# Performance work log

Measured on AMD Instinct MI355X. Metric: run time of the kernel, lower is better.

## Reference

```python
import jax, jax.numpy as jnp
import numpy as np

B, Q, H = 1, 2048, 2048
NH, NKV, HD = 16, 8, 128
PAST = 2048
EPS = 1e-6


def rotate_half(x):
    x1, x2 = x[..., : x.shape[-1] // 2], x[..., x.shape[-1] // 2 :]
    return jnp.concatenate((-x2, x1), axis=-1)


def rms_norm(x, w, eps=EPS):
    var = jnp.mean(jnp.square(x.astype(jnp.float32)), axis=-1, keepdims=True)
    return (x * jax.lax.rsqrt(var + eps)) * w


def setup_inputs() -> dict:
    key = jax.random.key(0)
    ks = jax.random.split(key, 8)
    hidden_states = jax.random.normal(ks[0], (B, Q, H), jnp.float32)
    # RoPE tables for positions [PAST, PAST+Q)
    inv_freq = 1.0 / (1000000.0 ** (np.arange(0, HD, 2, dtype=np.float32) / HD))
    pos = np.arange(PAST, PAST + Q, dtype=np.float32)
    freqs = np.outer(pos, inv_freq)  # [Q, HD/2]
    emb = np.concatenate([freqs, freqs], axis=-1)  # [Q, HD]
    cos = jnp.asarray(np.cos(emb))[None].repeat(B, 0)
    sin = jnp.asarray(np.sin(emb))[None].repeat(B, 0)
    # causal additive mask over kv_len = PAST + Q
    q_idx = np.arange(Q)[:, None] + PAST
    kv_idx = np.arange(PAST + Q)[None, :]
    mask = np.where(kv_idx <= q_idx, 0.0, -1e9).astype(np.float32)
    attention_mask = jnp.asarray(mask)[None, None]  # [1,1,Q,PAST+Q]
    s = 1.0 / np.sqrt(H)
    return {
        "hidden_states": hidden_states,
        "cos": cos,
        "sin": sin,
        "attention_mask": attention_mask,
        "past_key": jax.random.normal(ks[1], (B, NKV, PAST, HD), jnp.float32),
        "past_value": jax.random.normal(ks[2], (B, NKV, PAST, HD), jnp.float32),
        "Wq": jax.random.normal(ks[3], (NH * HD, H), jnp.float32) * s,
        "Wk": jax.random.normal(ks[4], (NKV * HD, H), jnp.float32) * s,
        "Wv": jax.random.normal(ks[5], (NKV * HD, H), jnp.float32) * s,
        "Wo": jax.random.normal(ks[6], (NH * HD, NH * HD), jnp.float32) * s,
        "q_norm_w": jnp.ones((HD,), jnp.float32),
        "k_norm_w": jnp.ones((HD,), jnp.float32),
    }


def reference(hidden_states, cos, sin, attention_mask, past_key, past_value,
              Wq, Wk, Wv, Wo, q_norm_w, k_norm_w):
    bsz, q_len, _ = hidden_states.shape
    scaling = HD ** -0.5
    n_rep = NH // NKV

    q = jnp.einsum("bsh,dh->bsd", hidden_states, Wq).reshape(bsz, q_len, NH, HD).transpose(0, 2, 1, 3)
    k = jnp.einsum("bsh,dh->bsd", hidden_states, Wk).reshape(bsz, q_len, NKV, HD).transpose(0, 2, 1, 3)
    v = jnp.einsum("bsh,dh->bsd", hidden_states, Wv).reshape(bsz, q_len, NKV, HD).transpose(0, 2, 1, 3)

    q = rms_norm(q, q_norm_w)
    k = rms_norm(k, k_norm_w)

    c = cos[:, None]  # [B,1,Q,HD]
    s = sin[:, None]
    q = q * c + rotate_half(q) * s
    k = k * c + rotate_half(k) * s

    k_all = jnp.concatenate([past_key, k], axis=2)    # [B,NKV,PAST+Q,HD]
    v_all = jnp.concatenate([past_value, v], axis=2)
    new_key = k_all[:, :, -q_len:, :]
    new_value = v_all[:, :, -q_len:, :]

    kv_len = k_all.shape[2]
    k_rep = jnp.broadcast_to(k_all[:, :, None], (bsz, NKV, n_rep, kv_len, HD)).reshape(bsz, NH, kv_len, HD)
    v_rep = jnp.broadcast_to(v_all[:, :, None], (bsz, NKV, n_rep, kv_len, HD)).reshape(bsz, NH, kv_len, HD)

    scores = jnp.einsum("bhqd,bhkd->bhqk", q, k_rep) * scaling + attention_mask
    probs = jax.nn.softmax(scores.astype(jnp.float32), axis=-1).astype(q.dtype)
    out = jnp.einsum("bhqk,bhkd->bhqd", probs, v_rep)
    out = out.transpose(0, 2, 1, 3).reshape(bsz, q_len, NH * HD)
    out = jnp.einsum("bsd,hd->bsh", out, Wo)
    return out, new_key, new_value
```

## Files before the change

kernel.cpp:

```cpp
#include <hip/hip_runtime.h>
#include <hip/hip_bf16.h>

typedef __bf16 bf16_t;
typedef __bf16 bf16x8 __attribute__((ext_vector_type(8)));
typedef float f32x4 __attribute__((ext_vector_type(4)));

#define NH 16
#define NKV 8
#define HD 128
#define QLEN 2048
#define PASTLEN 2048
#define KVLEN 4096
#define NKOFF 4194304UL
#define NVOFF 6291456UL
#define SM_C1 0.12751741f
#define SM_C2 (-28.853900817779268f)

__device__ __forceinline__ void async16(const void* g, void* l) {
  __builtin_amdgcn_global_load_lds(
      (const __attribute__((address_space(1))) unsigned int*)g,
      (__attribute__((address_space(3))) unsigned int*)l, 16, 0, 0);
}

__device__ __forceinline__ bool detect_f32(const void* qw) {
  return *(const unsigned*)qw == 0x3F800000u;
}

__device__ __forceinline__ float ld1(const void* p, size_t i, bool f32) {
  return f32 ? ((const float*)p)[i] : (float)((const bf16_t*)p)[i];
}
__device__ __forceinline__ void st1(void* p, size_t i, bool f32, float v) {
  if (f32) ((float*)p)[i] = v; else ((bf16_t*)p)[i] = (bf16_t)v;
}
template <bool F32>
__device__ __forceinline__ uint4 ld8cvt(const void* p, size_t i) {
  if constexpr (!F32) {
    return *(const uint4*)((const bf16_t*)p + i);
  } else {
    const float* f = (const float*)p + i;
    float4 f0 = *(const float4*)f;
    float4 f1 = *(const float4*)(f + 4);
    union { bf16_t h[8]; uint4 u; } r;
    r.h[0] = (bf16_t)f0.x; r.h[1] = (bf16_t)f0.y; r.h[2] = (bf16_t)f0.z; r.h[3] = (bf16_t)f0.w;
    r.h[4] = (bf16_t)f1.x; r.h[5] = (bf16_t)f1.y; r.h[6] = (bf16_t)f1.z; r.h[7] = (bf16_t)f1.w;
    return r.u;
  }
}
__device__ __forceinline__ unsigned bfbits(float v) {
  bf16_t h = (bf16_t)v;
  union { bf16_t h; unsigned short u; } x; x.h = h;
  return (unsigned)x.u;
}

__global__ __launch_bounds__(256) void k_cvt4(
    const float* __restrict__ s0, const float* __restrict__ s1,
    const float* __restrict__ s2, const float* __restrict__ s3,
    bf16_t* __restrict__ d0, bf16_t* __restrict__ d1,
    bf16_t* __restrict__ d2, bf16_t* __restrict__ d3,
    const void* __restrict__ qw)
{
  if (!detect_f32(qw)) return;
  const int ten = blockIdx.y;
  const float* s; bf16_t* d; size_t n;
  switch (ten) {
    case 0:  s = s0; d = d0; n = 4194304; break;
    case 1:  s = s1; d = d1; n = 4194304; break;
    case 2:  s = s2; d = d2; n = 2097152; break;
    default: s = s3; d = d3; n = 2097152; break;
  }
  const size_t i = ((size_t)blockIdx.x * 256 + threadIdx.x) * 8;
  if (i >= n) return;
  uint4 v = ld8cvt<true>(s, i);
  *(uint4*)(d + i) = v;
}
__global__ __launch_bounds__(256) void k_cvt1(
    const float* __restrict__ s, bf16_t* __restrict__ d, const void* __restrict__ qw)
{
  if (!detect_f32(qw)) return;
  const size_t i = ((size_t)blockIdx.x * 256 + threadIdx.x) * 8;
  uint4 v = ld8cvt<true>(s, i);
  *(uint4*)(d + i) = v;
}

__device__ __forceinline__ void gemm_acc(
    const bf16_t* __restrict__ A, const bf16_t* __restrict__ B,
    int lda, int ldb, int m0, int n0, int K,
    bf16_t (*As)[4096], bf16_t (*Bs)[4096], f32x4 (*acc)[4])
{
  const int tid  = threadIdx.x;
  const int lane = tid & 63;
  const int w    = tid >> 6;
  const int wm   = w >> 1, wn = w & 1;
  const int qid  = lane & 15, quad = lane >> 4;

  const int r4 = tid >> 2;
  const int sg = (tid & 3) * 8;
  const size_t a0 = (size_t)(m0 + r4) * lda + sg;
  const size_t a1 = a0 + (size_t)64 * lda;
  const size_t b0 = (size_t)(n0 + r4) * ldb + sg;
  const size_t b1 = b0 + (size_t)64 * ldb;
  const int lo0 = tid * 8;
  const int lo1 = 2048 + tid * 8;

  auto stage = [&](int k0, int buf) {
    async16(A + a0 + k0, As[buf] + lo0);
    async16(A + a1 + k0, As[buf] + lo1);
    async16(B + b0 + k0, Bs[buf] + lo0);
    async16(B + b1 + k0, Bs[buf] + lo1);
  };

  stage(0, 0);

  for (int k0 = 0; k0 < K; k0 += 32) {
    const int cur = (k0 >> 5) & 1;
    if (k0 + 32 < K) {
      stage(k0 + 32, cur ^ 1);
      asm volatile("s_waitcnt vmcnt(4)" ::: "memory");
    } else {
      asm volatile("s_waitcnt vmcnt(0)" ::: "memory");
    }
    __builtin_amdgcn_s_barrier();

    bf16x8 af[4], bfr[4];
#pragma unroll
    for (int i = 0; i < 4; i++)
      af[i] = *(const bf16x8*)(As[cur] + (size_t)(wm * 64 + i * 16 + qid) * 32 + quad * 8);
#pragma unroll
    for (int j = 0; j < 4; j++)
      bfr[j] = *(const bf16x8*)(Bs[cur] + (size_t)(wn * 64 + j * 16 + qid) * 32 + quad * 8);
#pragma unroll
    for (int i = 0; i < 4; i++)
#pragma unroll
      for (int j = 0; j < 4; j++)
        acc[i][j] = __builtin_amdgcn_mfma_f32_16x16x32_bf16(af[i], bfr[j], acc[i][j], 0, 0, 0);

    __builtin_amdgcn_s_barrier();
  }
}

__global__ __launch_bounds__(256) void k_gemm_qkv(
    const void* __restrict__ hs, const void* __restrict__ Wq,
    const void* __restrict__ Wk, const void* __restrict__ Wv,
    const bf16_t* __restrict__ hsb, const bf16_t* __restrict__ Wqb,
    const bf16_t* __restrict__ Wkb, const bf16_t* __restrict__ Wvb,
    const void* __restrict__ cs, const void* __restrict__ sn,
    const void* __restrict__ qw, const void* __restrict__ kw,
    bf16_t* __restrict__ qb, bf16_t* __restrict__ kc, void* __restrict__ dout)
{
  __shared__ __align__(16) char smem[67072];
  bf16_t (*As)[4096] = (bf16_t(*)[4096])smem;
  bf16_t (*Bs)[4096] = (bf16_t(*)[4096])(smem + 16384);
  float (*xs)[129]   = (float(*)[129])smem;
  float (*rsum)[128] = (float(*)[128])(smem + 66048);

  const bool f = detect_f32(qw);
  const bf16_t* A = f ? hsb : (const bf16_t*)hs;
  const int bx = blockIdx.x, by = blockIdx.y;
  const bf16_t* B; int n0;
  if (bx < 16)      { B = f ? Wqb : (const bf16_t*)Wq; n0 = bx * 128; }
  else if (bx < 24) { B = f ? Wkb : (const bf16_t*)Wk; n0 = (bx - 16) * 128; }
  else              { B = f ? Wvb : (const bf16_t*)Wv; n0 = (bx - 24) * 128; }

  f32x4 acc[4][4] = {};
  gemm_acc(A, B, 2048, 2048, by * 128, n0, 2048, As, Bs, acc);

  const int tid = threadIdx.x, lane = tid & 63, w = tid >> 6;
  const int wm = w >> 1, wn = w & 1, qid = lane & 15, quad = lane >> 4;

  if (bx >= 24) {
    const int h = bx - 24;
#pragma unroll
    for (int i = 0; i < 4; i++)
#pragma unroll
      for (int j = 0; j < 4; j++) {
        const int rl = wm * 64 + i * 16 + quad * 4;
        const int d  = wn * 64 + j * 16 + qid;
#pragma unroll
        for (int r = 0; r < 4; r++) {
          const int s = by * 128 + rl + r;
          st1(dout, NVOFF + ((size_t)h * QLEN + s) * HD + d, f, acc[i][j][r]);
        }
      }
    return;
  }

  float rs[4][4];
#pragma unroll
  for (int i = 0; i < 4; i++)
#pragma unroll
    for (int r = 0; r < 4; r++) {
      float v = 0.f;
#pragma unroll
      for (int j = 0; j < 4; j++) v += acc[i][j][r] * acc[i][j][r];
#pragma unroll
      for (int o = 1; o < 16; o <<= 1) v += __shfl_xor(v, o, 64);
      rs[i][r] = v;
    }
#pragma unroll
  for (int i = 0; i < 4; i++)
#pragma unroll
    for (int j = 0; j < 4; j++) {
      const int rl = wm * 64 + i * 16 + quad * 4;
      const int d  = wn * 64 + j * 16 + qid;
#pragma unroll
      for (int r = 0; r < 4; r++) xs[rl + r][d] = acc[i][j][r];
    }
  if (qid == 0) {
#pragma unroll
    for (int i = 0; i < 4; i++)
#pragma unroll
      for (int r = 0; r < 4; r++)
        rsum[wn][wm * 64 + i * 16 + quad * 4 + r] = rs[i][r];
  }
  __syncthreads();
  const void* wgt = (bx < 16) ? qw : kw;
#pragma unroll
  for (int i = 0; i < 4; i++)
#pragma unroll
    for (int r = 0; r < 4; r++) {
      const int rl = wm * 64 + i * 16 + quad * 4 + r;
      const int s  = by * 128 + rl;
      const float inv = rsqrtf((rsum[0][rl] + rsum[1][rl]) * (1.0f / 128.0f) + 1e-6f);
#pragma unroll
      for (int j = 0; j < 4; j++) {
        const int d = wn * 64 + j * 16 + qid;
        const float x  = acc[i][j][r];
        const float xp = xs[rl][d ^ 64];
        const float y  = x  * inv * ld1(wgt, d, f);
        const float yp = xp * inv * ld1(wgt, d ^ 64, f);
        const float cv = ld1(cs, (size_t)s * HD + d, f);
        const float sv = ld1(sn, (size_t)s * HD + d, f);
        const float o  = (d < 64) ? y * cv - yp * sv : y * cv + yp * sv;
        if (bx < 16) {
          qb[(size_t)s * 2048 + bx * HD + d] = (bf16_t)o;
        } else {
          const int hk = bx - 16;
          st1(dout, NKOFF + ((size_t)hk * QLEN + s) * HD + d, f, o);
          kc[((size_t)hk * KVLEN + PASTLEN + s) * HD + d] = (bf16_t)o;
        }
      }
    }
}

__global__ __launch_bounds__(256) void k_gemm_o(
    const bf16_t* __restrict__ aout, const void* __restrict__ Wo,
    const bf16_t* __restrict__ Wob, void* __restrict__ dout,
    const void* __restrict__ qw)
{
  __shared__ bf16_t As[2][4096];
  __shared__ bf16_t Bs[2][4096];
  const bool f = detect_f32(qw);
  const bf16_t* B = f ? Wob : (const bf16_t*)Wo;
  f32x4 acc[4][4] = {};
  gemm_acc(aout, B, 2048, 2048, blockIdx.y * 128, blockIdx.x * 128, 2048, As, Bs, acc);

  const int tid = threadIdx.x, lane = tid & 63, w = tid >> 6;
  const int wm = w >> 1, wn = w & 1, qid = lane & 15, quad = lane >> 4;
#pragma unroll
  for (int i = 0; i < 4; i++)
#pragma unroll
    for (int j = 0; j < 4; j++) {
      const int rr = blockIdx.y * 128 + wm * 64 + i * 16 + quad * 4;
      const int cc = blockIdx.x * 128 + wn * 64 + j * 16 + qid;
#pragma unroll
      for (int r = 0; r < 4; r++)
        st1(dout, (size_t)(rr + r) * 2048 + cc, f, acc[i][j][r]);
    }
}

template <bool F>
__device__ __forceinline__ void prep_body(
    const void* __restrict__ pk, const void* __restrict__ pv,
    const void* __restrict__ dout,
    bf16_t* __restrict__ kc, bf16_t* __restrict__ vt,
    unsigned (*tile)[65])
{
  const int tid = threadIdx.x;
  const int hk = blockIdx.x >> 5, kvt = blockIdx.x & 31;
  const int kv0 = kvt * 128;

  if (kv0 < PASTLEN) {
    const size_t base = ((size_t)hk * PASTLEN + kv0) * HD;
    bf16_t* dst = kc + ((size_t)hk * KVLEN + kv0) * HD;
#pragma unroll
    for (int p = 0; p < 8; p++) {
      const int id = p * 256 + tid;
      const int r = id >> 4, c8 = (id & 15) * 8;
      uint4 vv = ld8cvt<F>(pk, base + (size_t)r * HD + c8);
      *(uint4*)(dst + (size_t)r * HD + c8) = vv;
    }
  }

  const void* src; size_t base;
  if (kv0 < PASTLEN) { src = pv;   base = ((size_t)hk * PASTLEN + kv0) * HD; }
  else               { src = dout; base = NVOFF + ((size_t)hk * QLEN + (kv0 - PASTLEN)) * HD; }
#pragma unroll
  for (int p = 0; p < 4; p++) {
    const int id = p * 256 + tid;
    const int r = id >> 4, e8 = (id & 15) * 8;
    if constexpr (!F) {
      uint4 a = *(const uint4*)((const bf16_t*)src + base + (size_t)(2 * r) * HD + e8);
      uint4 b = *(const uint4*)((const bf16_t*)src + base + (size_t)(2 * r + 1) * HD + e8);
      unsigned av[4] = {a.x, a.y, a.z, a.w}, bv[4] = {b.x, b.y, b.z, b.w};
#pragma unroll
      for (int q = 0; q < 4; q++) {
        tile[e8 + 2 * q][r]     = (av[q] & 0xffffu) | (bv[q] << 16);
        tile[e8 + 2 * q + 1][r] = (av[q] >> 16)     | (bv[q] & 0xffff0000u);
      }
    } else {
      const float* fa = (const float*)src + base + (size_t)(2 * r) * HD + e8;
      const float* fb = (const float*)src + base + (size_t)(2 * r + 1) * HD + e8;
#pragma unroll
      for (int e = 0; e < 8; e++)
        tile[e8 + e][r] = bfbits(fa[e]) | (bfbits(fb[e]) << 16);
    }
  }
  __syncthreads();
#pragma unroll
  for (int p = 0; p < 8; p++) {
    const int id = p * 256 + tid;
    const int e = id >> 4, c4 = (id & 15) * 4;
    uint4 wv;
    if (c4 & 8) {
      wv.x = tile[e][c4 + 2]; wv.y = tile[e][c4 + 3]; wv.z = tile[e][c4];     wv.w = tile[e][c4 + 1];
    } else {
      wv.x = tile[e][c4];     wv.y = tile[e][c4 + 1]; wv.z = tile[e][c4 + 2]; wv.w = tile[e][c4 + 3];
    }
    *(uint4*)(vt + ((size_t)hk * HD + e) * KVLEN + kv0 + c4 * 2) = wv;
  }
}
__global__ __launch_bounds__(256) void k_prep_kv(
    const void* __restrict__ pk, const void* __restrict__ pv,
    const void* __restrict__ dout,
    bf16_t* __restrict__ kc, bf16_t* __restrict__ vt, const void* __restrict__ qw)
{
  __shared__ unsigned tile[128][65];
  if (detect_f32(qw)) prep_body<true>(pk, pv, dout, kc, vt, tile);
  else                prep_body<false>(pk, pv, dout, kc, vt, tile);
}

__global__ __launch_bounds__(256, 2) void k_attn(
    const bf16_t* __restrict__ qb, const bf16_t* __restrict__ kc,
    const bf16_t* __restrict__ vt, bf16_t* __restrict__ aout)
{
  __shared__ bf16_t ks[2][64 * 128];
  __shared__ bf16_t vs[2][128 * 64];
  __shared__ float  lsx[2][64];

  const int tid = threadIdx.x, lane = tid & 63, w = tid >> 6;
  const int qid = lane & 15, quad = lane >> 4;
  const int qg = w & 1;
  const int kh = w >> 1;
  const int bx = blockIdx.x;
  const int h  = ((bx & 7) << 1) | (bx >> 3);
  const int hk = h >> 1;
  const int by = blockIdx.y;
  const int qt = (by < 16) ? by : 47 - by;
  const int q0 = qt * 64;

  bf16x8 qf[2][4];
#pragma unroll
  for (int i = 0; i < 2; i++)
#pragma unroll
    for (int kst = 0; kst < 4; kst++)
      qf[i][kst] = *(const bf16x8*)(qb + (size_t)(q0 + qg * 32 + i * 16 + qid) * 2048
                                       + h * HD + kst * 32 + quad * 8);

  f32x4 Oacc[2][8] = {};
  f32x4 lacc[2] = {};

  union { unsigned short u[8]; bf16x8 v; } onesu;
#pragma unroll
  for (int e = 0; e < 8; e++) onesu.u[e] = 0x3F80;
  const bf16x8 onesv = onesu.v;

  const int J = quad >> 1;
  int bpa[4];
#pragma unroll
  for (int s = 0; s < 4; s++)
    bpa[s] = 4 * (qid + 16 * ((2 * quad + ((s >> 1) ^ J)) & 3));

  const bf16_t* kbase = kc + (size_t)hk * KVLEN * HD;
  const bf16_t* vbase = vt + (size_t)hk * HD * KVLEN;
  const int r16 = tid >> 4, ksg = tid & 15;
  const int r8  = tid >> 3, vsg = tid & 7;
  const int nt = qt + 33;

  auto stage = [&](int t, int buf) {
    const int kv0 = t * 64;
#pragma unroll
    for (int c = 0; c < 4; c++) {
      const int kr = c * 16 + r16;
      async16(kbase + (size_t)(kv0 + kr) * HD + ((ksg ^ (kr & 7)) * 8),
              &ks[buf][(size_t)(c * 256 + tid) * 8]);
    }
#pragma unroll
    for (int c = 0; c < 4; c++) {
      const int vr = c * 32 + r8;
      async16(vbase + (size_t)vr * KVLEN + kv0 + ((vsg ^ (vr & 7)) * 8),
              &vs[buf][(size_t)(c * 256 + tid) * 8]);
    }
  };

  stage(0, 0);

  for (int t = 0; t < nt; ++t) {
    const int cur = t & 1;
    if (t + 1 < nt) {
      stage(t + 1, cur ^ 1);
      asm volatile("s_waitcnt vmcnt(8)" ::: "memory");
    } else {
      asm volatile("s_waitcnt vmcnt(0)" ::: "memory");
    }
    __builtin_amdgcn_s_barrier();

    const bf16_t* ksb = ks[cur];
    const bf16_t* vsb = vs[cur];
    const int kv0 = t * 64;

    f32x4 sf[2][2] = {};
    __builtin_amdgcn_s_setprio(1);
#pragma unroll
    for (int kst = 0; kst < 4; kst++) {
      bf16x8 kf[2];
#pragma unroll
      for (int j = 0; j < 2; j++)
        kf[j] = *(const bf16x8*)(ksb + (size_t)((kh * 2 + j) * 16 + qid) * 128
                                     + (((kst * 4 + quad) * 8) ^ ((qid & 7) * 8)));
#pragma unroll
      for (int i = 0; i < 2; i++)
#pragma unroll
        for (int j = 0; j < 2; j++)
          sf[i][j] = __builtin_amdgcn_mfma_f32_16x16x32_bf16(kf[j], qf[i][kst], sf[i][j], 0, 0, 0);
    }
    __builtin_amdgcn_s_setprio(0);

    const bool lastt = (t == nt - 1);
    bf16x8 pf[2];
#pragma unroll
    for (int i = 0; i < 2; i++) {
      const int qglob = q0 + qg * 32 + i * 16 + qid + PASTLEN;
      float pr[2][4];
#pragma unroll
      for (int j = 0; j < 2; j++) {
        const int kvb = kv0 + kh * 32 + j * 16 + quad * 4;
#pragma unroll
        for (int r = 0; r < 4; r++) {
          float v = fmaf(sf[i][j][r], SM_C1, SM_C2);
          if (lastt && (kvb + r) > qglob) v = -1e9f;
          pr[j][r] = exp2f(v);
        }
      }
      unsigned pk00, pk01, pk10, pk11;
      asm("v_cvt_pk_bf16_f32 %0, %1, %2" : "=v"(pk00) : "v"(pr[0][0]), "v"(pr[0][1]));
      asm("v_cvt_pk_bf16_f32 %0, %1, %2" : "=v"(pk01) : "v"(pr[0][2]), "v"(pr[0][3]));
      asm("v_cvt_pk_bf16_f32 %0, %1, %2" : "=v"(pk10) : "v"(pr[1][0]), "v"(pr[1][1]));
      asm("v_cvt_pk_bf16_f32 %0, %1, %2" : "=v"(pk11) : "v"(pr[1][2]), "v"(pr[1][3]));
      const bool qodd = (quad & 1) != 0;
      const unsigned reg0 = qodd ? pk10 : pk00;
      const unsigned reg1 = qodd ? pk11 : pk01;
      const unsigned reg2 = qodd ? pk00 : pk10;
      const unsigned reg3 = qodd ? pk01 : pk11;
      union { unsigned u[4]; bf16x8 v; } pu;
      pu.u[0] = (unsigned)__builtin_amdgcn_ds_bpermute(bpa[0], (int)reg0);
      pu.u[1] = (unsigned)__builtin_amdgcn_ds_bpermute(bpa[1], (int)reg1);
      pu.u[2] = (unsigned)__builtin_amdgcn_ds_bpermute(bpa[2], (int)reg2);
      pu.u[3] = (unsigned)__builtin_amdgcn_ds_bpermute(bpa[3], (int)reg3);
      pf[i] = pu.v;
    }

    __builtin_amdgcn_s_setprio(1);
    lacc[0] = __builtin_amdgcn_mfma_f32_16x16x32_bf16(pf[0], onesv, lacc[0], 0, 0, 0);
    lacc[1] = __builtin_amdgcn_mfma_f32_16x16x32_bf16(pf[1], onesv, lacc[1], 0, 0, 0);
#pragma unroll
    for (int n = 0; n < 8; n++) {
      bf16x8 vf = *(const bf16x8*)(vsb + (size_t)(n * 16 + qid) * 64
                                       + (((kh * 4 + quad) * 8) ^ ((qid & 7) * 8)));
      Oacc[0][n] = __builtin_amdgcn_mfma_f32_16x16x32_bf16(pf[0], vf, Oacc[0][n], 0, 0, 0);
      Oacc[1][n] = __builtin_amdgcn_mfma_f32_16x16x32_bf16(pf[1], vf, Oacc[1][n], 0, 0, 0);
    }
    __builtin_amdgcn_s_setprio(0);
    __builtin_amdgcn_s_barrier();
  }

  if (qid == 0) {
#pragma unroll
    for (int i = 0; i < 2; i++)
#pragma unroll
      for (int r = 0; r < 4; r++)
        lsx[kh][qg * 32 + i * 16 + quad * 4 + r] = lacc[i][r];
  }
  float* Osc = (float*)ks;
  if (kh == 1) {
#pragma unroll
    for (int i = 0; i < 2; i++)
#pragma unroll
      for (int n = 0; n < 8; n++)
#pragma unroll
        for (int r = 0; r < 4; r++)
          Osc[(size_t)qg * 4096 + (i * 16 + quad * 4 + r) * 128 + n * 16 + qid] = Oacc[i][n][r];
  }
  __syncthreads();
  if (kh == 0) {
#pragma unroll
    for (int i = 0; i < 2; i++) {
      float invl[4];
#pragma unroll
      for (int r = 0; r < 4; r++) {
        const int qq = qg * 32 + i * 16 + quad * 4 + r;
        invl[r] = 1.0f / (lsx[0][qq] + lsx[1][qq]);
      }
#pragma unroll
      for (int n = 0; n < 8; n++)
#pragma unroll
        for (int r = 0; r < 4; r++) {
          const float ot = Oacc[i][n][r]
            + Osc[(size_t)qg * 4096 + (i * 16 + quad * 4 + r) * 128 + n * 16 + qid];
          const int row = q0 + qg * 32 + i * 16 + quad * 4 + r;
          aout[(size_t)row * 2048 + h * HD + n * 16 + qid] = (bf16_t)(ot * invl[r]);
        }
    }
  }
}

extern "C" void kernel_launch(void* const* d_in, const int* in_sizes, int n_in,
                              void* d_out, int out_size, void* d_ws, size_t ws_size,
                              hipStream_t stream) {
  const void* hs = d_in[0];
  const void* cs = d_in[1];
  const void* sn = d_in[2];
  const void* pk = d_in[4];
  const void* pv = d_in[5];
  const void* Wq = d_in[6];
  const void* Wk = d_in[7];
  const void* Wv = d_in[8];
  const void* Wo = d_in[9];
  const void* qw = d_in[10];
  const void* kw = d_in[11];

  char* ws = (char*)d_ws;
  bf16_t* qb   = (bf16_t*)(ws);
  bf16_t* kc   = (bf16_t*)(ws + (size_t)8  * 1024 * 1024);
  bf16_t* hsb  = (bf16_t*)(ws + (size_t)16 * 1024 * 1024);
  bf16_t* vt   = (bf16_t*)(ws + (size_t)16 * 1024 * 1024);
  bf16_t* Wqb  = (bf16_t*)(ws + (size_t)24 * 1024 * 1024);
  bf16_t* aout = (bf16_t*)(ws + (size_t)24 * 1024 * 1024);
  bf16_t* Wkb  = (bf16_t*)(ws + (size_t)32 * 1024 * 1024);
  bf16_t* Wvb  = (bf16_t*)(ws + (size_t)36 * 1024 * 1024);
  bf16_t* Wob  = (bf16_t*)(ws + (size_t)32 * 1024 * 1024);

  hipLaunchKernelGGL(k_cvt4, dim3(2048, 4), dim3(256), 0, stream,
                     (const float*)hs, (const float*)Wq, (const float*)Wk, (const float*)Wv,
                     hsb, Wqb, Wkb, Wvb, qw);
  hipLaunchKernelGGL(k_gemm_qkv, dim3(32, 16), dim3(256), 0, stream,
                     hs, Wq, Wk, Wv, hsb, Wqb, Wkb, Wvb, cs, sn, qw, kw, qb, kc, d_out);
  hipLaunchKernelGGL(k_cvt1, dim3(2048), dim3(256), 0, stream, (const float*)Wo, Wob, qw);
  hipLaunchKernelGGL(k_prep_kv, dim3(256), dim3(256), 0, stream, pk, pv, d_out, kc, vt, qw);
  hipLaunchKernelGGL(k_attn, dim3(16, 32), dim3(256), 0, stream, qb, kc, vt, aout);
  hipLaunchKernelGGL(k_gemm_o, dim3(16, 16), dim3(256), 0, stream, aout, Wo, Wob, d_out, qw);
}
```

Before: 381.4 us.

## Enlarge GEMM tiles to 256x128x64 with swizzled LDS and compute attention row sums in VALU

The shared GEMM mainloop now runs 512-thread blocks on a 256x128 output tile with a 64-wide K step. Global-to-LDS loads use an XOR swizzle to avoid bank conflicts, and the MFMA section runs at raised wave priority. This halves the grid for the QKV and output projections and improves operand reuse per load. The cost is larger LDS use, and the output GEMM only fills 128 blocks. The QKV epilogue stages its RoPE partner values in LDS as bf16 instead of fp32, which slightly lowers precision. The attention kernel computes softmax row sums with scalar adds and shuffles instead of extra MFMAs against a ones vector.

```diff
diff --git a/kernel.cpp b/kernel.cpp
--- a/kernel.cpp
+++ b/kernel.cpp
@@ -85,7 +85,7 @@
 __device__ __forceinline__ void gemm_acc(
     const bf16_t* __restrict__ A, const bf16_t* __restrict__ B,
     int lda, int ldb, int m0, int n0, int K,
-    bf16_t (*As)[4096], bf16_t (*Bs)[4096], f32x4 (*acc)[4])
+    bf16_t (*As)[16384], bf16_t (*Bs)[8192], f32x4 (*acc)[4])
 {
   const int tid  = threadIdx.x;
   const int lane = tid & 63;
@@ -93,52 +93,62 @@
   const int wm   = w >> 1, wn = w & 1;
   const int qid  = lane & 15, quad = lane >> 4;
 
-  const int r4 = tid >> 2;
-  const int sg = (tid & 3) * 8;
-  const size_t a0 = (size_t)(m0 + r4) * lda + sg;
-  const size_t a1 = a0 + (size_t)64 * lda;
-  const size_t b0 = (size_t)(n0 + r4) * ldb + sg;
-  const size_t b1 = b0 + (size_t)64 * ldb;
-  const int lo0 = tid * 8;
-  const int lo1 = 2048 + tid * 8;
-
-  auto stage = [&](int k0, int buf) {
-    async16(A + a0 + k0, As[buf] + lo0);
-    async16(A + a1 + k0, As[buf] + lo1);
-    async16(B + b0 + k0, Bs[buf] + lo0);
-    async16(B + b1 + k0, Bs[buf] + lo1);
+  auto stage = [&](int kt, int buf) {
+    const int k0 = kt * 64;
+#pragma unroll
+    for (int c = 0; c < 4; c++) {
+      const int id = c * 512 + tid;
+      const int row = id >> 3, segp = id & 7;
+      async16(A + (size_t)(m0 + row) * lda + k0 + ((segp ^ (row & 7)) * 8),
+              As[buf] + (size_t)id * 8);
+    }
+#pragma unroll
+    for (int c = 0; c < 2; c++) {
+      const int id = c * 512 + tid;
+      const int row = id >> 3, segp = id & 7;
+      async16(B + (size_t)(n0 + row) * ldb + k0 + ((segp ^ (row & 7)) * 8),
+              Bs[buf] + (size_t)id * 8);
+    }
   };
 
   stage(0, 0);
-
-  for (int k0 = 0; k0 < K; k0 += 32) {
-    const int cur = (k0 >> 5) & 1;
-    if (k0 + 32 < K) {
-      stage(k0 + 32, cur ^ 1);
-      asm volatile("s_waitcnt vmcnt(4)" ::: "memory");
+  const int NT = K >> 6;
+  for (int kt = 0; kt < NT; kt++) {
+    const int cur = kt & 1;
+    if (kt + 1 < NT) {
+      stage(kt + 1, cur ^ 1);
+      asm volatile("s_waitcnt vmcnt(6)" ::: "memory");
     } else {
       asm volatile("s_waitcnt vmcnt(0)" ::: "memory");
     }
     __builtin_amdgcn_s_barrier();
 
-    bf16x8 af[4], bfr[4];
-#pragma unroll
-    for (int i = 0; i < 4; i++)
-      af[i] = *(const bf16x8*)(As[cur] + (size_t)(wm * 64 + i * 16 + qid) * 32 + quad * 8);
-#pragma unroll
-    for (int j = 0; j < 4; j++)
-      bfr[j] = *(const bf16x8*)(Bs[cur] + (size_t)(wn * 64 + j * 16 + qid) * 32 + quad * 8);
-#pragma unroll
-    for (int i = 0; i < 4; i++)
-#pragma unroll
-      for (int j = 0; j < 4; j++)
-        acc[i][j] = __builtin_amdgcn_mfma_f32_16x16x32_bf16(af[i], bfr[j], acc[i][j], 0, 0, 0);
-
+    __builtin_amdgcn_s_setprio(1);
+#pragma unroll
+    for (int ks = 0; ks < 2; ks++) {
+      bf16x8 bfr[4];
+#pragma unroll
+      for (int j = 0; j < 4; j++) {
+        const int row = wn * 64 + j * 16 + qid;
+        bfr[j] = *(const bf16x8*)(Bs[cur] + (size_t)row * 64
+                                         + (((ks * 4 + quad) ^ (row & 7)) * 8));
+      }
+#pragma unroll
+      for (int i = 0; i < 4; i++) {
+        const int row = wm * 64 + i * 16 + qid;
+        bf16x8 af = *(const bf16x8*)(As[cur] + (size_t)row * 64
+                                            + (((ks * 4 + quad) ^ (row & 7)) * 8));
+#pragma unroll
+        for (int j = 0; j < 4; j++)
+          acc[i][j] = __builtin_amdgcn_mfma_f32_16x16x32_bf16(af, bfr[j], acc[i][j], 0, 0, 0);
+      }
+    }
+    __builtin_amdgcn_s_setprio(0);
     __builtin_amdgcn_s_barrier();
   }
 }
 
-__global__ __launch_bounds__(256) void k_gemm_qkv(
+__global__ __launch_bounds__(512, 2) void k_gemm_qkv(
     const void* __restrict__ hs, const void* __restrict__ Wq,
     const void* __restrict__ Wk, const void* __restrict__ Wv,
     const bf16_t* __restrict__ hsb, const bf16_t* __restrict__ Wqb,
@@ -147,11 +157,11 @@
     const void* __restrict__ qw, const void* __restrict__ kw,
     bf16_t* __restrict__ qb, bf16_t* __restrict__ kc, void* __restrict__ dout)
 {
-  __shared__ __align__(16) char smem[67072];
-  bf16_t (*As)[4096] = (bf16_t(*)[4096])smem;
-  bf16_t (*Bs)[4096] = (bf16_t(*)[4096])(smem + 16384);
-  float (*xs)[129]   = (float(*)[129])smem;
-  float (*rsum)[128] = (float(*)[128])(smem + 66048);
+  __shared__ __align__(16) char smem[98304];
+  bf16_t (*As)[16384] = (bf16_t(*)[16384])smem;
+  bf16_t (*Bs)[8192]  = (bf16_t(*)[8192])(smem + 65536);
+  bf16_t* xsb  = (bf16_t*)smem;
+  float*  rsum = (float*)(smem + 67584);
 
   const bool f = detect_f32(qw);
   const bf16_t* A = f ? hsb : (const bf16_t*)hs;
@@ -162,7 +172,7 @@
   else              { B = f ? Wvb : (const bf16_t*)Wv; n0 = (bx - 24) * 128; }
 
   f32x4 acc[4][4] = {};
-  gemm_acc(A, B, 2048, 2048, by * 128, n0, 2048, As, Bs, acc);
+  gemm_acc(A, B, 2048, 2048, by * 256, n0, 2048, As, Bs, acc);
 
   const int tid = threadIdx.x, lane = tid & 63, w = tid >> 6;
   const int wm = w >> 1, wn = w & 1, qid = lane & 15, quad = lane >> 4;
@@ -177,14 +187,13 @@
         const int d  = wn * 64 + j * 16 + qid;
 #pragma unroll
         for (int r = 0; r < 4; r++) {
-          const int s = by * 128 + rl + r;
+          const int s = by * 256 + rl + r;
           st1(dout, NVOFF + ((size_t)h * QLEN + s) * HD + d, f, acc[i][j][r]);
         }
       }
     return;
   }
 
-  float rs[4][4];
 #pragma unroll
   for (int i = 0; i < 4; i++)
 #pragma unroll
@@ -194,40 +203,42 @@
       for (int j = 0; j < 4; j++) v += acc[i][j][r] * acc[i][j][r];
 #pragma unroll
       for (int o = 1; o < 16; o <<= 1) v += __shfl_xor(v, o, 64);
-      rs[i][r] = v;
-    }
-#pragma unroll
-  for (int i = 0; i < 4; i++)
+      if (qid == 0) rsum[wn * 256 + wm * 64 + i * 16 + quad * 4 + r] = v;
+    }
+#pragma unroll
+  for (int i = 0; i < 4; i++) {
+    const int rlb = wm * 64 + i * 16 + quad * 4;
 #pragma unroll
     for (int j = 0; j < 4; j++) {
-      const int rl = wm * 64 + i * 16 + quad * 4;
-      const int d  = wn * 64 + j * 16 + qid;
-#pragma unroll
-      for (int r = 0; r < 4; r++) xs[rl + r][d] = acc[i][j][r];
-    }
-  if (qid == 0) {
-#pragma unroll
-    for (int i = 0; i < 4; i++)
-#pragma unroll
-      for (int r = 0; r < 4; r++)
-        rsum[wn][wm * 64 + i * 16 + quad * 4 + r] = rs[i][r];
+      const int d = wn * 64 + j * 16 + qid;
+      union { bf16_t h[4]; unsigned long long u; } px;
+#pragma unroll
+      for (int r = 0; r < 4; r++) px.h[r] = (bf16_t)acc[i][j][r];
+      *(unsigned long long*)(xsb + (size_t)d * 264 + rlb) = px.u;
+    }
   }
   __syncthreads();
   const void* wgt = (bx < 16) ? qw : kw;
 #pragma unroll
-  for (int i = 0; i < 4; i++)
-#pragma unroll
-    for (int r = 0; r < 4; r++) {
-      const int rl = wm * 64 + i * 16 + quad * 4 + r;
-      const int s  = by * 128 + rl;
-      const float inv = rsqrtf((rsum[0][rl] + rsum[1][rl]) * (1.0f / 128.0f) + 1e-6f);
-#pragma unroll
-      for (int j = 0; j < 4; j++) {
-        const int d = wn * 64 + j * 16 + qid;
+  for (int i = 0; i < 4; i++) {
+    const int rlb = wm * 64 + i * 16 + quad * 4;
+    float inv[4];
+#pragma unroll
+    for (int r = 0; r < 4; r++)
+      inv[r] = rsqrtf((rsum[rlb + r] + rsum[256 + rlb + r]) * (1.0f / 128.0f) + 1e-6f);
+#pragma unroll
+    for (int j = 0; j < 4; j++) {
+      const int d = wn * 64 + j * 16 + qid;
+      const float wv  = ld1(wgt, d, f);
+      const float wvp = ld1(wgt, d ^ 64, f);
+      union { bf16_t h[4]; unsigned long long u; } xp;
+      xp.u = *(const unsigned long long*)(xsb + (size_t)(d ^ 64) * 264 + rlb);
+#pragma unroll
+      for (int r = 0; r < 4; r++) {
+        const int s = by * 256 + rlb + r;
         const float x  = acc[i][j][r];
-        const float xp = xs[rl][d ^ 64];
-        const float y  = x  * inv * ld1(wgt, d, f);
-        const float yp = xp * inv * ld1(wgt, d ^ 64, f);
+        const float y  = x * inv[r] * wv;
+        const float yp = (float)xp.h[r] * inv[r] * wvp;
         const float cv = ld1(cs, (size_t)s * HD + d, f);
         const float sv = ld1(sn, (size_t)s * HD + d, f);
         const float o  = (d < 64) ? y * cv - yp * sv : y * cv + yp * sv;
@@ -240,19 +251,21 @@
         }
       }
     }
-}
-
-__global__ __launch_bounds__(256) void k_gemm_o(
+  }
+}
+
+__global__ __launch_bounds__(512, 2) void k_gemm_o(
     const bf16_t* __restrict__ aout, const void* __restrict__ Wo,
     const bf16_t* __restrict__ Wob, void* __restrict__ dout,
     const void* __restrict__ qw)
 {
-  __shared__ bf16_t As[2][4096];
-  __shared__ bf16_t Bs[2][4096];
+  __shared__ __align__(16) char smem[98304];
+  bf16_t (*As)[16384] = (bf16_t(*)[16384])smem;
+  bf16_t (*Bs)[8192]  = (bf16_t(*)[8192])(smem + 65536);
   const bool f = detect_f32(qw);
   const bf16_t* B = f ? Wob : (const bf16_t*)Wo;
   f32x4 acc[4][4] = {};
-  gemm_acc(aout, B, 2048, 2048, blockIdx.y * 128, blockIdx.x * 128, 2048, As, Bs, acc);
+  gemm_acc(aout, B, 2048, 2048, blockIdx.y * 256, blockIdx.x * 128, 2048, As, Bs, acc);
 
   const int tid = threadIdx.x, lane = tid & 63, w = tid >> 6;
   const int wm = w >> 1, wn = w & 1, qid = lane & 15, quad = lane >> 4;
@@ -260,7 +273,7 @@
   for (int i = 0; i < 4; i++)
 #pragma unroll
     for (int j = 0; j < 4; j++) {
-      const int rr = blockIdx.y * 128 + wm * 64 + i * 16 + quad * 4;
+      const int rr = blockIdx.y * 256 + wm * 64 + i * 16 + quad * 4;
       const int cc = blockIdx.x * 128 + wn * 64 + j * 16 + qid;
 #pragma unroll
       for (int r = 0; r < 4; r++)
@@ -367,12 +380,7 @@
                                        + h * HD + kst * 32 + quad * 8);
 
   f32x4 Oacc[2][8] = {};
-  f32x4 lacc[2] = {};
-
-  union { unsigned short u[8]; bf16x8 v; } onesu;
-#pragma unroll
-  for (int e = 0; e < 8; e++) onesu.u[e] = 0x3F80;
-  const bf16x8 onesv = onesu.v;
+  float lsum[2] = {0.f, 0.f};
 
   const int J = quad >> 1;
   int bpa[4];
@@ -448,7 +456,9 @@
         for (int r = 0; r < 4; r++) {
           float v = fmaf(sf[i][j][r], SM_C1, SM_C2);
           if (lastt && (kvb + r) > qglob) v = -1e9f;
-          pr[j][r] = exp2f(v);
+          const float p = exp2f(v);
+          lsum[i] += p;
+          pr[j][r] = p;
         }
       }
       unsigned pk00, pk01, pk10, pk11;
@@ -470,8 +480,6 @@
     }
 
     __builtin_amdgcn_s_setprio(1);
-    lacc[0] = __builtin_amdgcn_mfma_f32_16x16x32_bf16(pf[0], onesv, lacc[0], 0, 0, 0);
-    lacc[1] = __builtin_amdgcn_mfma_f32_16x16x32_bf16(pf[1], onesv, lacc[1], 0, 0, 0);
 #pragma unroll
     for (int n = 0; n < 8; n++) {
       bf16x8 vf = *(const bf16x8*)(vsb + (size_t)(n * 16 + qid) * 64
@@ -483,12 +491,14 @@
     __builtin_amdgcn_s_barrier();
   }
 
-  if (qid == 0) {
-#pragma unroll
-    for (int i = 0; i < 2; i++)
-#pragma unroll
-      for (int r = 0; r < 4; r++)
-        lsx[kh][qg * 32 + i * 16 + quad * 4 + r] = lacc[i][r];
+#pragma unroll
+  for (int i = 0; i < 2; i++) {
+    lsum[i] += __shfl_xor(lsum[i], 16, 64);
+    lsum[i] += __shfl_xor(lsum[i], 32, 64);
+  }
+  if (quad == 0) {
+    lsx[kh][qg * 32 + qid]      = lsum[0];
+    lsx[kh][qg * 32 + 16 + qid] = lsum[1];
   }
   float* Osc = (float*)ks;
   if (kh == 1) {
@@ -552,10 +562,10 @@
   hipLaunchKernelGGL(k_cvt4, dim3(2048, 4), dim3(256), 0, stream,
                      (const float*)hs, (const float*)Wq, (const float*)Wk, (const float*)Wv,
                      hsb, Wqb, Wkb, Wvb, qw);
-  hipLaunchKernelGGL(k_gemm_qkv, dim3(32, 16), dim3(256), 0, stream,
+  hipLaunchKernelGGL(k_gemm_qkv, dim3(32, 8), dim3(512), 0, stream,
                      hs, Wq, Wk, Wv, hsb, Wqb, Wkb, Wvb, cs, sn, qw, kw, qb, kc, d_out);
   hipLaunchKernelGGL(k_cvt1, dim3(2048), dim3(256), 0, stream, (const float*)Wo, Wob, qw);
   hipLaunchKernelGGL(k_prep_kv, dim3(256), dim3(256), 0, stream, pk, pv, d_out, kc, vt, qw);
   hipLaunchKernelGGL(k_attn, dim3(16, 32), dim3(256), 0, stream, qb, kc, vt, aout);
-  hipLaunchKernelGGL(k_gemm_o, dim3(16, 16), dim3(256), 0, stream, aout, Wo, Wob, d_out, qw);
-}
+  hipLaunchKernelGGL(k_gemm_o, dim3(16, 8), dim3(512), 0, stream, aout, Wo, Wob, d_out, qw);
+}
```

Result: faster. 366.4 us (-3.9%).

## Deepen GEMM K tile to 64 with swizzled LDS; scalar softmax row sums

Applied to the files above, without the earlier changes.

The shared GEMM routine now stages 64-wide K tiles with an XOR-swizzled LDS layout, so fragment reads avoid bank conflicts. It splits each tile into two 32-wide halves with the B prefetch issued between them, and raises MFMA priority around the math. This halves the number of barrier and wait rounds per K sweep, but it doubles the LDS footprint, which may lower occupancy in the output projection. In attention, the softmax denominator is now summed in fp32 registers with cross-lane shuffles, replacing the extra MFMA against a ones vector.

```diff
diff --git a/kernel.cpp b/kernel.cpp
--- a/kernel.cpp
+++ b/kernel.cpp
@@ -85,7 +85,7 @@
 __device__ __forceinline__ void gemm_acc(
     const bf16_t* __restrict__ A, const bf16_t* __restrict__ B,
     int lda, int ldb, int m0, int n0, int K,
-    bf16_t (*As)[4096], bf16_t (*Bs)[4096], f32x4 (*acc)[4])
+    bf16_t (*As)[8192], bf16_t (*Bs)[8192], f32x4 (*acc)[4])
 {
   const int tid  = threadIdx.x;
   const int lane = tid & 63;
@@ -93,47 +93,80 @@
   const int wm   = w >> 1, wn = w & 1;
   const int qid  = lane & 15, quad = lane >> 4;
 
-  const int r4 = tid >> 2;
-  const int sg = (tid & 3) * 8;
-  const size_t a0 = (size_t)(m0 + r4) * lda + sg;
-  const size_t a1 = a0 + (size_t)64 * lda;
-  const size_t b0 = (size_t)(n0 + r4) * ldb + sg;
-  const size_t b1 = b0 + (size_t)64 * ldb;
-  const int lo0 = tid * 8;
-  const int lo1 = 2048 + tid * 8;
-
-  auto stage = [&](int k0, int buf) {
-    async16(A + a0 + k0, As[buf] + lo0);
-    async16(A + a1 + k0, As[buf] + lo1);
-    async16(B + b0 + k0, Bs[buf] + lo0);
-    async16(B + b1 + k0, Bs[buf] + lo1);
+  const int srow = tid >> 3, ssegp = tid & 7;
+
+  auto stageA = [&](int kt, int buf) {
+#pragma unroll
+    for (int c = 0; c < 4; c++) {
+      const int row = c * 32 + srow;
+      async16(A + (size_t)(m0 + row) * lda + kt * 64 + ((ssegp ^ (row & 7)) * 8),
+              As[buf] + (size_t)(c * 256 + tid) * 8);
+    }
   };
-
-  stage(0, 0);
-
-  for (int k0 = 0; k0 < K; k0 += 32) {
-    const int cur = (k0 >> 5) & 1;
-    if (k0 + 32 < K) {
-      stage(k0 + 32, cur ^ 1);
+  auto stageB = [&](int kt, int buf) {
+#pragma unroll
+    for (int c = 0; c < 4; c++) {
+      const int row = c * 32 + srow;
+      async16(B + (size_t)(n0 + row) * ldb + kt * 64 + ((ssegp ^ (row & 7)) * 8),
+              Bs[buf] + (size_t)(c * 256 + tid) * 8);
+    }
+  };
+
+  stageA(0, 0); stageB(0, 0);
+  const int NT = K >> 6;
+  for (int kt = 0; kt < NT; kt++) {
+    const int cur = kt & 1;
+    if (kt + 1 < NT) {
+      stageA(kt + 1, cur ^ 1);
       asm volatile("s_waitcnt vmcnt(4)" ::: "memory");
     } else {
       asm volatile("s_waitcnt vmcnt(0)" ::: "memory");
     }
     __builtin_amdgcn_s_barrier();
 
-    bf16x8 af[4], bfr[4];
-#pragma unroll
-    for (int i = 0; i < 4; i++)
-      af[i] = *(const bf16x8*)(As[cur] + (size_t)(wm * 64 + i * 16 + qid) * 32 + quad * 8);
-#pragma unroll
-    for (int j = 0; j < 4; j++)
-      bfr[j] = *(const bf16x8*)(Bs[cur] + (size_t)(wn * 64 + j * 16 + qid) * 32 + quad * 8);
-#pragma unroll
-    for (int i = 0; i < 4; i++)
-#pragma unroll
-      for (int j = 0; j < 4; j++)
-        acc[i][j] = __builtin_amdgcn_mfma_f32_16x16x32_bf16(af[i], bfr[j], acc[i][j], 0, 0, 0);
-
+    {
+      bf16x8 af[4], bfr[4];
+#pragma unroll
+      for (int j = 0; j < 4; j++) {
+        const int row = wn * 64 + j * 16 + qid;
+        bfr[j] = *(const bf16x8*)(Bs[cur] + (size_t)row * 64 + ((quad ^ (row & 7)) * 8));
+      }
+#pragma unroll
+      for (int i = 0; i < 4; i++) {
+        const int row = wm * 64 + i * 16 + qid;
+        af[i] = *(const bf16x8*)(As[cur] + (size_t)row * 64 + ((quad ^ (row & 7)) * 8));
+      }
+      __builtin_amdgcn_s_setprio(1);
+#pragma unroll
+      for (int i = 0; i < 4; i++)
+#pragma unroll
+        for (int j = 0; j < 4; j++)
+          acc[i][j] = __builtin_amdgcn_mfma_f32_16x16x32_bf16(af[i], bfr[j], acc[i][j], 0, 0, 0);
+      __builtin_amdgcn_s_setprio(0);
+    }
+    if (kt + 1 < NT) stageB(kt + 1, cur ^ 1);
+    __builtin_amdgcn_s_barrier();
+
+    {
+      bf16x8 af[4], bfr[4];
+#pragma unroll
+      for (int j = 0; j < 4; j++) {
+        const int row = wn * 64 + j * 16 + qid;
+        bfr[j] = *(const bf16x8*)(Bs[cur] + (size_t)row * 64 + (((4 + quad) ^ (row & 7)) * 8));
+      }
+#pragma unroll
+      for (int i = 0; i < 4; i++) {
+        const int row = wm * 64 + i * 16 + qid;
+        af[i] = *(const bf16x8*)(As[cur] + (size_t)row * 64 + (((4 + quad) ^ (row & 7)) * 8));
+      }
+      __builtin_amdgcn_s_setprio(1);
+#pragma unroll
+      for (int i = 0; i < 4; i++)
+#pragma unroll
+        for (int j = 0; j < 4; j++)
+          acc[i][j] = __builtin_amdgcn_mfma_f32_16x16x32_bf16(af[i], bfr[j], acc[i][j], 0, 0, 0);
+      __builtin_amdgcn_s_setprio(0);
+    }
     __builtin_amdgcn_s_barrier();
   }
 }
@@ -148,8 +181,8 @@
     bf16_t* __restrict__ qb, bf16_t* __restrict__ kc, void* __restrict__ dout)
 {
   __shared__ __align__(16) char smem[67072];
-  bf16_t (*As)[4096] = (bf16_t(*)[4096])smem;
-  bf16_t (*Bs)[4096] = (bf16_t(*)[4096])(smem + 16384);
+  bf16_t (*As)[8192] = (bf16_t(*)[8192])smem;
+  bf16_t (*Bs)[8192] = (bf16_t(*)[8192])(smem + 32768);
   float (*xs)[129]   = (float(*)[129])smem;
   float (*rsum)[128] = (float(*)[128])(smem + 66048);
 
@@ -247,8 +280,9 @@
     const bf16_t* __restrict__ Wob, void* __restrict__ dout,
     const void* __restrict__ qw)
 {
-  __shared__ bf16_t As[2][4096];
-  __shared__ bf16_t Bs[2][4096];
+  __shared__ __align__(16) char smem[65536];
+  bf16_t (*As)[8192] = (bf16_t(*)[8192])smem;
+  bf16_t (*Bs)[8192] = (bf16_t(*)[8192])(smem + 32768);
   const bool f = detect_f32(qw);
   const bf16_t* B = f ? Wob : (const bf16_t*)Wo;
   f32x4 acc[4][4] = {};
@@ -367,12 +401,7 @@
                                        + h * HD + kst * 32 + quad * 8);
 
   f32x4 Oacc[2][8] = {};
-  f32x4 lacc[2] = {};
-
-  union { unsigned short u[8]; bf16x8 v; } onesu;
-#pragma unroll
-  for (int e = 0; e < 8; e++) onesu.u[e] = 0x3F80;
-  const bf16x8 onesv = onesu.v;
+  float lsum[2] = {0.f, 0.f};
 
   const int J = quad >> 1;
   int bpa[4];
@@ -448,7 +477,9 @@
         for (int r = 0; r < 4; r++) {
           float v = fmaf(sf[i][j][r], SM_C1, SM_C2);
           if (lastt && (kvb + r) > qglob) v = -1e9f;
-          pr[j][r] = exp2f(v);
+          const float p = exp2f(v);
+          lsum[i] += p;
+          pr[j][r] = p;
         }
       }
       unsigned pk00, pk01, pk10, pk11;
@@ -470,8 +501,6 @@
     }
 
     __builtin_amdgcn_s_setprio(1);
-    lacc[0] = __builtin_amdgcn_mfma_f32_16x16x32_bf16(pf[0], onesv, lacc[0], 0, 0, 0);
-    lacc[1] = __builtin_amdgcn_mfma_f32_16x16x32_bf16(pf[1], onesv, lacc[1], 0, 0, 0);
 #pragma unroll
     for (int n = 0; n < 8; n++) {
       bf16x8 vf = *(const bf16x8*)(vsb + (size_t)(n * 16 + qid) * 64
@@ -483,12 +512,14 @@
     __builtin_amdgcn_s_barrier();
   }
 
-  if (qid == 0) {
-#pragma unroll
-    for (int i = 0; i < 2; i++)
-#pragma unroll
-      for (int r = 0; r < 4; r++)
-        lsx[kh][qg * 32 + i * 16 + quad * 4 + r] = lacc[i][r];
+#pragma unroll
+  for (int i = 0; i < 2; i++) {
+    lsum[i] += __shfl_xor(lsum[i], 16, 64);
+    lsum[i] += __shfl_xor(lsum[i], 32, 64);
+  }
+  if (quad == 0) {
+    lsx[kh][qg * 32 + qid]      = lsum[0];
+    lsx[kh][qg * 32 + 16 + qid] = lsum[1];
   }
   float* Osc = (float*)ks;
   if (kh == 1) {
```

New measurement: 362.4 us. -5.0%, faster.
